# Optimization experiments

Hardware: AMD Instinct MI355X
Metric: run time of the kernel (lower is better)

The kernel has to match this reference:

```python
import jax, jax.numpy as jnp
import numpy as np

B, T, D, H, L = 32, 2048, 512, 512, 2
G = 4 * H


def _lstm_layer(x, h0, c0, Wih, Whh, bih, bhh):
    """Run one LSTM layer over time, vectorized across batch.

    x: [B, T, D_in]; h0, c0: [H] (shared initial state across batch, as in the
    original module where every batch element reuses the same `states[i]`).
    Returns (ys [B, T, H], hT [B, H], cT [B, H]).
    """
    b = x.shape[0]
    # Precompute the input contribution to the gates for all timesteps at once
    # (the only part that doesn't depend on the recurrence): [B, T, 4H]
    xg = jnp.einsum('btd,gd->btg', x, Wih) + (bih + bhh)
    h_init = jnp.broadcast_to(h0, (b, H))
    c_init = jnp.broadcast_to(c0, (b, H))

    def step(carry, xg_t):
        h, c = carry  # [B, H] each
        gates = xg_t + h @ Whh.T  # [B, 4H]
        i, f, g, o = jnp.split(gates, 4, axis=-1)  # torch LSTMCell gate order
        c = jax.nn.sigmoid(f) * c + jax.nn.sigmoid(i) * jnp.tanh(g)
        h = jax.nn.sigmoid(o) * jnp.tanh(c)
        return (h, c), h

    (hT, cT), ys = jax.lax.scan(step, (h_init, c_init), jnp.swapaxes(xg, 0, 1))
    return jnp.swapaxes(ys, 0, 1), hT, cT  # ys -> [B, T, H]


def setup_inputs() -> dict:
    key = jax.random.key(0)
    ks = jax.random.split(key, 9)
    s_in = 1.0 / np.sqrt(H)
    inp = {
        'x': jax.random.normal(ks[0], (B, T, D), jnp.float32),
        'Wih0': jax.random.normal(ks[1], (G, D), jnp.float32) * s_in,
        'Whh0': jax.random.normal(ks[2], (G, H), jnp.float32) * s_in,
        'bih0': jax.random.normal(ks[3], (G,), jnp.float32) * s_in,
        'bhh0': jax.random.normal(ks[4], (G,), jnp.float32) * s_in,
        'Wih1': jax.random.normal(ks[5], (G, H), jnp.float32) * s_in,
        'Whh1': jax.random.normal(ks[6], (G, H), jnp.float32) * s_in,
        'bih1': jax.random.normal(ks[7], (G,), jnp.float32) * s_in,
        'bhh1': jax.random.normal(ks[8], (G,), jnp.float32) * s_in,
        'h0': jnp.zeros((L, H), jnp.float32),
        'c0': jnp.zeros((L, H), jnp.float32),
    }
    return inp


def reference(x, Wih0, Whh0, bih0, bhh0, Wih1, Whh1, bih1, bhh1, h0, c0):
    # Layer 0
    y, h_f0, c_f0 = _lstm_layer(x, h0[0], c0[0], Wih0, Whh0, bih0, bhh0)
    # Layer 1 (no dropout: dropout_probability=None)
    y, h_f1, c_f1 = _lstm_layer(y, h0[1], c0[1], Wih1, Whh1, bih1, bhh1)
    h_final = jnp.stack([h_f0, h_f1])  # [L, B, H]
    c_final = jnp.stack([c_f0, c_f1])  # [L, B, H]
    return y, h_final, c_final
```

## Files before the change

### kernel.cpp

```cpp
#include <hip/hip_runtime.h>

namespace {
constexpr int TT   = 2048;
constexpr int NBLK = 128;
constexpr size_t YSZ = (size_t)32 * TT * 512;
constexpr size_t HFO = YSZ;
constexpr size_t CFO = YSZ + (size_t)2 * 32 * 512;
}

typedef float f32x4 __attribute__((ext_vector_type(4)));
typedef short s16x8 __attribute__((ext_vector_type(8)));

__device__ __forceinline__ float sigf(float v)  { return 1.0f / (1.0f + __expf(-v)); }
__device__ __forceinline__ float tanh_(float v) { return 1.0f - 2.0f / (__expf(2.0f * v) + 1.0f); }
__device__ __forceinline__ short f2bf(float v) {
  unsigned u = __float_as_uint(v);
  u += 0x7FFFu + ((u >> 16) & 1u);
  return (short)(u >> 16);
}
__device__ __forceinline__ float bf2f(short h) {
  return __uint_as_float(((unsigned)(unsigned short)h) << 16);
}
__device__ __forceinline__ void st_short_coh(void* p, int v) {
  asm volatile("global_store_short %0, %1, off sc1" :: "v"(p), "v"(v) : "memory");
}
__device__ __forceinline__ void poll2(const int* f, int need) {
  while (true) {
    const int a = __hip_atomic_load(f,      __ATOMIC_RELAXED, __HIP_MEMORY_SCOPE_AGENT);
    const int b = __hip_atomic_load(f + 64, __ATOMIC_RELAXED, __HIP_MEMORY_SCOPE_AGENT);
    if (a >= need && b >= need) break;
    __builtin_amdgcn_s_sleep(1);
  }
}

#define GLLP(g, l) __builtin_amdgcn_global_load_lds(                          \
    (const __attribute__((address_space(1))) void*)(g),                       \
    (__attribute__((address_space(3))) void*)(l), 16, 0, 0)
#define GLLC(g, l) __builtin_amdgcn_global_load_lds(                          \
    (const __attribute__((address_space(1))) void*)(g),                       \
    (__attribute__((address_space(3))) void*)(l), 16, 0, 0x11)

#define VMCNT0() do { asm volatile("s_waitcnt vmcnt(0)" ::: "memory"); __builtin_amdgcn_sched_barrier(0); } while (0)
#define LGKM0()  do { asm volatile("s_waitcnt lgkmcnt(0)" ::: "memory"); __builtin_amdgcn_sched_barrier(0); } while (0)
#define BAR()    do { __builtin_amdgcn_s_barrier(); __builtin_amdgcn_sched_barrier(0); } while (0)

__global__ __launch_bounds__(512)
void lstm_persist(
    const float* __restrict__ x,
    const float* __restrict__ Wih0, const float* __restrict__ Whh0,
    const float* __restrict__ bih0, const float* __restrict__ bhh0,
    const float* __restrict__ Wih1, const float* __restrict__ Whh1,
    const float* __restrict__ bih1, const float* __restrict__ bhh1,
    const float* __restrict__ h0c, const float* __restrict__ c0c,
    float* __restrict__ out,
    short* __restrict__ r0hi, short* __restrict__ r0lo,
    short* __restrict__ r1hi, short* __restrict__ r1lo,
    int* __restrict__ flags0, int* __restrict__ flags1)
{
  __shared__ __align__(16) short Whi[16 * 1024];
  __shared__ __align__(16) short Wlo[16 * 1024];
  __shared__ __align__(16) float stage[32 * 512];
  __shared__ __align__(16) float gbuf[16 * 33];
  __shared__ __align__(16) float xgb[2][16 * 33];

  const int tid   = (int)threadIdx.x;
  const int layer = (int)(blockIdx.x >> 7);
  const int lb    = (int)(blockIdx.x & (NBLK - 1));
  const int j0    = lb << 2;
  const int lane  = tid & 63;
  const int wg    = tid >> 6;
  char* stageb = (char*)stage;

  const float* Wih = layer ? Wih1 : Wih0;
  const float* Whh = layer ? Whh1 : Whh0;
  const float* bih = layer ? bih1 : bih0;
  const float* bhh = layer ? bhh1 : bhh0;
  short* rwhi = layer ? r1hi : r0hi;
  short* rwlo = layer ? r1lo : r0lo;
  int* fl_own = layer ? flags1 : flags0;
  const int awb = layer ? 0 : 512;
  const int bwb = layer ? 512 : 0;

  for (int idx = tid; idx < 16 * 1024; idx += 512) {
    const int row = idx >> 10;
    const int k   = idx & 1023;
    const int rg  = ((row >> 2) << 9) + j0 + (row & 3);
    const float v = (k < 512) ? Wih[(rg << 9) + k] : Whh[(rg << 9) + (k - 512)];
    const short h = f2bf(v);
    const short l = f2bf(v - bf2f(h));
    const int byte = (row << 11) + ((k << 1) ^ ((row & 7) << 4));
    *(short*)((char*)Whi + byte) = h;
    *(short*)((char*)Wlo + byte) = l;
  }
  float creg = 0.0f;
  float bias_[4] = {0.f, 0.f, 0.f, 0.f};
  if (tid < 128) {
    const int jj = tid & 3;
    creg = c0c[layer * 512 + j0 + jj];
#pragma unroll
    for (int g = 0; g < 4; ++g) {
      const int rg = (g << 9) + j0 + jj;
      bias_[g] = bih[rg] + bhh[rg];
    }
  }

  auto stage_planes = [&](const short* rh, const short* rl) {
#pragma unroll
    for (int i = 0; i < 4; ++i) {
      const int b = (i << 3) + wg;
      const int off = (b << 10) + ((lane << 4) ^ ((b & 7) << 4));
      GLLC((const char*)rh + off, stageb + (b << 10));
      GLLC((const char*)rl + off, stageb + 32768 + (b << 10));
    }
  };
  auto stage_x = [&](int sn) {
#pragma unroll
    for (int i = 0; i < 8; ++i) {
      const int u = (wg << 3) + i;
      const int b = u >> 1, half = (u & 1) << 10;
      const char* src = (const char*)x + ((size_t)(b * 2048 + sn) << 11) + half
                        + ((lane << 4) ^ ((b & 7) << 4));
      GLLP(src, stageb + (b << 11) + half);
    }
  };
  auto stage_bcast = [&](const float* p) {
#pragma unroll
    for (int i = 0; i < 8; ++i) {
      const int u = (wg << 3) + i;
      const int b = u >> 1, half = (u & 1) << 10;
      GLLP((const char*)p + half + ((lane << 4) ^ ((b & 7) << 4)),
           stageb + (b << 11) + half);
    }
  };

  auto do_mfma = [&](int wbase, bool cvt, float* dst) {
    f32x4 a0 = {0.f, 0.f, 0.f, 0.f}, a1 = {0.f, 0.f, 0.f, 0.f};
    const int arow = lane & 15;
    const int kg   = lane >> 4;
    const int bb   = (wg << 4) + (lane & 15);
    const int wsz  = (arow & 7) << 4;
    const int usz  = (bb & 7) << 4;
#pragma unroll
    for (int ks = 0; ks < 16; ++ks) {
      const int ku = ks * 32 + (kg << 3);
      const int wb = ((wbase + ku) << 1) ^ wsz;
      const s16x8 ah = *(const s16x8*)((const char*)Whi + (arow << 11) + wb);
      const s16x8 al = *(const s16x8*)((const char*)Wlo + (arow << 11) + wb);
      s16x8 bh, bl;
      if (!cvt) {
        const int ub = ((ku << 1) ^ usz);
        bh = *(const s16x8*)(stageb + (bb << 10) + ub);
        bl = *(const s16x8*)(stageb + 32768 + (bb << 10) + ub);
      } else {
        const f32x4 p = *(const f32x4*)(stageb + (bb << 11) + ((ku << 2) ^ usz));
        const f32x4 q = *(const f32x4*)(stageb + (bb << 11) + (((ku + 4) << 2) ^ usz));
        const float pv[8] = {p.x, p.y, p.z, p.w, q.x, q.y, q.z, q.w};
#pragma unroll
        for (int j = 0; j < 8; ++j) {
          const short h = f2bf(pv[j]);
          bh[j] = h;
          bl[j] = f2bf(pv[j] - bf2f(h));
        }
      }
      if (ks & 1) {
        a1 = __builtin_amdgcn_mfma_f32_16x16x32_bf16(ah, bh, a1, 0, 0, 0);
        a1 = __builtin_amdgcn_mfma_f32_16x16x32_bf16(ah, bl, a1, 0, 0, 0);
        a1 = __builtin_amdgcn_mfma_f32_16x16x32_bf16(al, bh, a1, 0, 0, 0);
      } else {
        a0 = __builtin_amdgcn_mfma_f32_16x16x32_bf16(ah, bh, a0, 0, 0, 0);
        a0 = __builtin_amdgcn_mfma_f32_16x16x32_bf16(ah, bl, a0, 0, 0, 0);
        a0 = __builtin_amdgcn_mfma_f32_16x16x32_bf16(al, bh, a0, 0, 0, 0);
      }
    }
    const f32x4 c = a0 + a1;
#pragma unroll
    for (int r = 0; r < 4; ++r)
      dst[((kg << 2) + r) * 33 + (wg << 4) + (lane & 15)] = c[r];
    LGKM0();
  };

  VMCNT0(); LGKM0(); BAR();

  if (layer == 0) stage_x(0); else stage_bcast(h0c + 512);
  VMCNT0(); BAR();
  if (wg < 2) do_mfma(bwb, true, &xgb[0][0]);
  if (layer == 1 && wg == 2) poll2(flags0 + lane, 1);
  BAR();
  if (layer == 0) stage_bcast(h0c);
  else            stage_planes(r0hi, r0lo);
  VMCNT0(); BAR();

#pragma unroll 1
  for (int s = 0; s < TT; ++s) {
    const int slot = s & 3;
    if (wg < 2) do_mfma(awb, layer == 0 && s == 0, gbuf);
    if (tid < 128) {
      const int jj = tid & 3;
      const int b  = tid >> 2;
      const float* xg = &xgb[s & 1][0];
      const float gi = gbuf[jj * 33 + b]        + xg[jj * 33 + b]        + bias_[0];
      const float gf = gbuf[(4 + jj) * 33 + b]  + xg[(4 + jj) * 33 + b]  + bias_[1];
      const float gg = gbuf[(8 + jj) * 33 + b]  + xg[(8 + jj) * 33 + b]  + bias_[2];
      const float go = gbuf[(12 + jj) * 33 + b] + xg[(12 + jj) * 33 + b] + bias_[3];
      const float cn = sigf(gf) * creg + sigf(gi) * tanh_(gg);
      const float hn = sigf(go) * tanh_(cn);
      creg = cn;
      const int j = j0 + jj;
      const short hb = f2bf(hn);
      const short lbh = f2bf(hn - bf2f(hb));
      short* ph = rwhi + (((slot << 5) + b) << 9) + j;
      short* pl = rwlo + (((slot << 5) + b) << 9) + j;
      st_short_coh(ph, (int)hb);
      st_short_coh(pl, (int)lbh);
      if (layer == 1) out[((size_t)((b << 11) + s) << 9) + j] = hn;
      if (s == TT - 1) out[HFO + (size_t)(((layer << 5) + b) << 9) + j] = hn;
      asm volatile("s_waitcnt vmcnt(0)" ::: "memory");
    }
    __builtin_amdgcn_sched_barrier(0);
    BAR();
    if (tid == 0)
      __hip_atomic_store(fl_own + lb, s + 1, __ATOMIC_RELAXED, __HIP_MEMORY_SCOPE_AGENT);

    if (s + 1 < TT) {
      if (layer == 1) {
        if (wg == 2) poll2(flags1 + lane, s + 1);
        BAR();
      }
      if (layer == 0) stage_x(s + 1);
      else            stage_planes(r1hi + (slot << 14), r1lo + (slot << 14));
      VMCNT0(); BAR();
      if (wg < 2) do_mfma(bwb, layer == 0, &xgb[(s + 1) & 1][0]);
      if (wg == 2) poll2(flags0 + lane, layer == 0 ? s + 1 : s + 2);
      if (wg == 3 && s >= 3) poll2(flags1 + lane, s - 2);
      BAR();
      if (layer == 0) stage_planes(r0hi + (slot << 14), r0lo + (slot << 14));
      else            stage_planes(r0hi + (((s + 1) & 3) << 14), r0lo + (((s + 1) & 3) << 14));
      VMCNT0(); BAR();
    }
  }

  if (tid < 128)
    out[CFO + (size_t)(((layer << 5) + (tid >> 2)) << 9) + j0 + (tid & 3)] = creg;
}

extern "C" void kernel_launch(void* const* d_in, const int* in_sizes, int n_in,
                              void* d_out, int out_size, void* d_ws, size_t ws_size,
                              hipStream_t stream) {
  (void)in_sizes; (void)n_in; (void)out_size; (void)ws_size;
  const float* x    = (const float*)d_in[0];
  const float* Wih0 = (const float*)d_in[1];
  const float* Whh0 = (const float*)d_in[2];
  const float* bih0 = (const float*)d_in[3];
  const float* bhh0 = (const float*)d_in[4];
  const float* Wih1 = (const float*)d_in[5];
  const float* Whh1 = (const float*)d_in[6];
  const float* bih1 = (const float*)d_in[7];
  const float* bhh1 = (const float*)d_in[8];
  const float* h0   = (const float*)d_in[9];
  const float* c0   = (const float*)d_in[10];

  float* out = (float*)d_out;
  short* r0hi = (short*)d_ws;
  short* r0lo = (short*)((char*)d_ws + (128 << 10));
  short* r1hi = (short*)((char*)d_ws + (256 << 10));
  short* r1lo = (short*)((char*)d_ws + (384 << 10));
  int* flags0 = (int*)((char*)d_ws + (512 << 10));
  int* flags1 = (int*)((char*)d_ws + (512 << 10) + 512);

  hipMemsetAsync(flags0, 0, 1024, stream);

  hipLaunchKernelGGL(lstm_persist, dim3(2 * NBLK), dim3(512), 0, stream,
                     x, Wih0, Whh0, bih0, bhh0, Wih1, Whh1, bih1, bhh1,
                     h0, c0, out, r0hi, r0lo, r1hi, r1lo, flags0, flags1);
}
```

Measured before the change: 16.70 ms.

## Split block into recurrent and input-projection wave groups with chunked double-buffered staging

Restructures the persistent LSTM kernel into 256-thread blocks where two waves compute only the recurrent h@Whh MFMA and two other waves compute the input projection and the gate nonlinearities. The input-projection waves stream x (or the layer-0 h planes) in eight k-chunks with double buffering and partial vmcnt waits, so loads overlap MFMA work. Per-wave flags replace per-block flags, which shortens the critical recurrent path. This raises LDS use to about 148KB and makes the synchronisation more intricate, with risk of added polling overhead.

```diff
diff --git a/kernel.cpp b/kernel.cpp
--- a/kernel.cpp
+++ b/kernel.cpp
@@ -6,6 +6,12 @@
 constexpr size_t YSZ = (size_t)32 * TT * 512;
 constexpr size_t HFO = YSZ;
 constexpr size_t CFO = YSZ + (size_t)2 * 32 * 512;
+constexpr int O_WLO = 32768;
+constexpr int O_AST = 65536;
+constexpr int O_B0  = 131072;
+constexpr int O_B1  = 139264;
+constexpr int O_GA  = 147456;
+constexpr int O_XGB = 149568;
 }
 
 typedef float f32x4 __attribute__((ext_vector_type(4)));
@@ -24,12 +30,20 @@
 __device__ __forceinline__ void st_short_coh(void* p, int v) {
   asm volatile("global_store_short %0, %1, off sc1" :: "v"(p), "v"(v) : "memory");
 }
-__device__ __forceinline__ void poll2(const int* f, int need) {
-  while (true) {
-    const int a = __hip_atomic_load(f,      __ATOMIC_RELAXED, __HIP_MEMORY_SCOPE_AGENT);
-    const int b = __hip_atomic_load(f + 64, __ATOMIC_RELAXED, __HIP_MEMORY_SCOPE_AGENT);
-    if (a >= need && b >= need) break;
+__device__ __forceinline__ void st_flag(int* p, int v) {
+  __hip_atomic_store(p, v, __ATOMIC_RELAXED, __HIP_MEMORY_SCOPE_AGENT);
+}
+__device__ __forceinline__ void poll_ge(const int* f, int need) {
+  while (__hip_atomic_load(f, __ATOMIC_RELAXED, __HIP_MEMORY_SCOPE_AGENT) < need)
     __builtin_amdgcn_s_sleep(1);
+}
+__device__ __forceinline__ void cvt8(const f32x4& p, const f32x4& q, s16x8& bh, s16x8& bl) {
+  const float pv[8] = {p.x, p.y, p.z, p.w, q.x, q.y, q.z, q.w};
+#pragma unroll
+  for (int j = 0; j < 8; ++j) {
+    const short h = f2bf(pv[j]);
+    bh[j] = h;
+    bl[j] = f2bf(pv[j] - bf2f(h));
   }
 }
 
@@ -40,11 +54,12 @@
     (const __attribute__((address_space(1))) void*)(g),                       \
     (__attribute__((address_space(3))) void*)(l), 16, 0, 0x11)
 
+#define VMCNT4() do { asm volatile("s_waitcnt vmcnt(4)" ::: "memory"); __builtin_amdgcn_sched_barrier(0); } while (0)
 #define VMCNT0() do { asm volatile("s_waitcnt vmcnt(0)" ::: "memory"); __builtin_amdgcn_sched_barrier(0); } while (0)
 #define LGKM0()  do { asm volatile("s_waitcnt lgkmcnt(0)" ::: "memory"); __builtin_amdgcn_sched_barrier(0); } while (0)
 #define BAR()    do { __builtin_amdgcn_s_barrier(); __builtin_amdgcn_sched_barrier(0); } while (0)
 
-__global__ __launch_bounds__(512)
+__global__ __launch_bounds__(256)
 void lstm_persist(
     const float* __restrict__ x,
     const float* __restrict__ Wih0, const float* __restrict__ Whh0,
@@ -57,190 +72,229 @@
     short* __restrict__ r1hi, short* __restrict__ r1lo,
     int* __restrict__ flags0, int* __restrict__ flags1)
 {
-  __shared__ __align__(16) short Whi[16 * 1024];
-  __shared__ __align__(16) short Wlo[16 * 1024];
-  __shared__ __align__(16) float stage[32 * 512];
-  __shared__ __align__(16) float gbuf[16 * 33];
-  __shared__ __align__(16) float xgb[2][16 * 33];
+  __shared__ __align__(16) char LDS[151680];
+  char* Whi = LDS;
+  char* Wlo = LDS + O_WLO;
+  char* Ast = LDS + O_AST;
+  char* const Bst0 = LDS + O_B0;
+  char* const Bst1 = LDS + O_B1;
+  float* gA  = (float*)(LDS + O_GA);
+  float* xgb = (float*)(LDS + O_XGB);
 
   const int tid   = (int)threadIdx.x;
+  const int lane  = tid & 63;
+  const int w     = tid >> 6;
   const int layer = (int)(blockIdx.x >> 7);
   const int lb    = (int)(blockIdx.x & (NBLK - 1));
   const int j0    = lb << 2;
-  const int lane  = tid & 63;
-  const int wg    = tid >> 6;
-  char* stageb = (char*)stage;
+  const bool isA  = (w < 2);
 
   const float* Wih = layer ? Wih1 : Wih0;
   const float* Whh = layer ? Whh1 : Whh0;
   const float* bih = layer ? bih1 : bih0;
   const float* bhh = layer ? bhh1 : bhh0;
-  short* rwhi = layer ? r1hi : r0hi;
-  short* rwlo = layer ? r1lo : r0lo;
-  int* fl_own = layer ? flags1 : flags0;
-  const int awb = layer ? 0 : 512;
-  const int bwb = layer ? 512 : 0;
-
-  for (int idx = tid; idx < 16 * 1024; idx += 512) {
+  short* rhiO = layer ? r1hi : r0hi;
+  short* rloO = layer ? r1lo : r0lo;
+  int* flO = layer ? flags1 : flags0;
+
+  for (int idx = tid; idx < 16 * 1024; idx += 256) {
     const int row = idx >> 10;
     const int k   = idx & 1023;
     const int rg  = ((row >> 2) << 9) + j0 + (row & 3);
     const float v = (k < 512) ? Wih[(rg << 9) + k] : Whh[(rg << 9) + (k - 512)];
     const short h = f2bf(v);
     const short l = f2bf(v - bf2f(h));
-    const int byte = (row << 11) + ((k << 1) ^ ((row & 7) << 4));
-    *(short*)((char*)Whi + byte) = h;
-    *(short*)((char*)Wlo + byte) = l;
+    const int byte = (row << 11) + ((k << 1) ^ ((row & 15) << 4));
+    *(short*)(Whi + byte) = h;
+    *(short*)(Wlo + byte) = l;
   }
   float creg = 0.0f;
   float bias_[4] = {0.f, 0.f, 0.f, 0.f};
-  if (tid < 128) {
-    const int jj = tid & 3;
-    creg = c0c[layer * 512 + j0 + jj];
+  int jjC = 0, bC = 0;
+  if (!isA) {
+    jjC = lane >> 4;
+    bC  = ((w - 2) << 4) + (lane & 15);
+    creg = c0c[layer * 512 + j0 + jjC];
 #pragma unroll
     for (int g = 0; g < 4; ++g) {
-      const int rg = (g << 9) + j0 + jj;
+      const int rg = (g << 9) + j0 + jjC;
       bias_[g] = bih[rg] + bhh[rg];
     }
   }
 
-  auto stage_planes = [&](const short* rh, const short* rl) {
-#pragma unroll
-    for (int i = 0; i < 4; ++i) {
-      const int b = (i << 3) + wg;
-      const int off = (b << 10) + ((lane << 4) ^ ((b & 7) << 4));
-      GLLC((const char*)rh + off, stageb + (b << 10));
-      GLLC((const char*)rl + off, stageb + 32768 + (b << 10));
+  const int arow = lane & 15;
+  const int kg   = lane >> 4;
+  const int wsz  = arow << 4;
+  const int bbA  = (w << 4) + (lane & 15);
+  const int uszA = (bbA & 15) << 4;
+  const int bbB  = ((w - 2) << 4) + (lane & 15);
+  const int uszB  = (bbB & 15) << 4;
+  const int uszB7 = (bbB & 7) << 4;
+
+  if (isA) {
+    const char* src0 = (const char*)(h0c + layer * 512);
+#pragma unroll 1
+    for (int i = 0; i < 32; ++i) {
+      const int g = (w << 5) + i;
+      const int b = g >> 1, half = g & 1;
+      GLLP(src0 + (half << 10) + ((lane << 4) ^ ((b & 15) << 4)),
+           Ast + (b << 11) + (half << 10));
     }
-  };
-  auto stage_x = [&](int sn) {
-#pragma unroll
-    for (int i = 0; i < 8; ++i) {
-      const int u = (wg << 3) + i;
-      const int b = u >> 1, half = (u & 1) << 10;
-      const char* src = (const char*)x + ((size_t)(b * 2048 + sn) << 11) + half
-                        + ((lane << 4) ^ ((b & 7) << 4));
-      GLLP(src, stageb + (b << 11) + half);
-    }
-  };
-  auto stage_bcast = [&](const float* p) {
-#pragma unroll
-    for (int i = 0; i < 8; ++i) {
-      const int u = (wg << 3) + i;
-      const int b = u >> 1, half = (u & 1) << 10;
-      GLLP((const char*)p + half + ((lane << 4) ^ ((b & 7) << 4)),
-           stageb + (b << 11) + half);
-    }
-  };
-
-  auto do_mfma = [&](int wbase, bool cvt, float* dst) {
-    f32x4 a0 = {0.f, 0.f, 0.f, 0.f}, a1 = {0.f, 0.f, 0.f, 0.f};
-    const int arow = lane & 15;
-    const int kg   = lane >> 4;
-    const int bb   = (wg << 4) + (lane & 15);
-    const int wsz  = (arow & 7) << 4;
-    const int usz  = (bb & 7) << 4;
-#pragma unroll
-    for (int ks = 0; ks < 16; ++ks) {
-      const int ku = ks * 32 + (kg << 3);
-      const int wb = ((wbase + ku) << 1) ^ wsz;
-      const s16x8 ah = *(const s16x8*)((const char*)Whi + (arow << 11) + wb);
-      const s16x8 al = *(const s16x8*)((const char*)Wlo + (arow << 11) + wb);
-      s16x8 bh, bl;
-      if (!cvt) {
-        const int ub = ((ku << 1) ^ usz);
-        bh = *(const s16x8*)(stageb + (bb << 10) + ub);
-        bl = *(const s16x8*)(stageb + 32768 + (bb << 10) + ub);
-      } else {
-        const f32x4 p = *(const f32x4*)(stageb + (bb << 11) + ((ku << 2) ^ usz));
-        const f32x4 q = *(const f32x4*)(stageb + (bb << 11) + (((ku + 4) << 2) ^ usz));
-        const float pv[8] = {p.x, p.y, p.z, p.w, q.x, q.y, q.z, q.w};
-#pragma unroll
-        for (int j = 0; j < 8; ++j) {
-          const short h = f2bf(pv[j]);
-          bh[j] = h;
-          bl[j] = f2bf(pv[j] - bf2f(h));
-        }
-      }
-      if (ks & 1) {
-        a1 = __builtin_amdgcn_mfma_f32_16x16x32_bf16(ah, bh, a1, 0, 0, 0);
-        a1 = __builtin_amdgcn_mfma_f32_16x16x32_bf16(ah, bl, a1, 0, 0, 0);
-        a1 = __builtin_amdgcn_mfma_f32_16x16x32_bf16(al, bh, a1, 0, 0, 0);
-      } else {
-        a0 = __builtin_amdgcn_mfma_f32_16x16x32_bf16(ah, bh, a0, 0, 0, 0);
-        a0 = __builtin_amdgcn_mfma_f32_16x16x32_bf16(ah, bl, a0, 0, 0, 0);
-        a0 = __builtin_amdgcn_mfma_f32_16x16x32_bf16(al, bh, a0, 0, 0, 0);
-      }
-    }
-    const f32x4 c = a0 + a1;
-#pragma unroll
-    for (int r = 0; r < 4; ++r)
-      dst[((kg << 2) + r) * 33 + (wg << 4) + (lane & 15)] = c[r];
-    LGKM0();
-  };
-
-  VMCNT0(); LGKM0(); BAR();
-
-  if (layer == 0) stage_x(0); else stage_bcast(h0c + 512);
-  VMCNT0(); BAR();
-  if (wg < 2) do_mfma(bwb, true, &xgb[0][0]);
-  if (layer == 1 && wg == 2) poll2(flags0 + lane, 1);
+    VMCNT0();
+  }
   BAR();
-  if (layer == 0) stage_bcast(h0c);
-  else            stage_planes(r0hi, r0lo);
-  VMCNT0(); BAR();
 
 #pragma unroll 1
   for (int s = 0; s < TT; ++s) {
     const int slot = s & 3;
-    if (wg < 2) do_mfma(awb, layer == 0 && s == 0, gbuf);
-    if (tid < 128) {
-      const int jj = tid & 3;
-      const int b  = tid >> 2;
-      const float* xg = &xgb[s & 1][0];
-      const float gi = gbuf[jj * 33 + b]        + xg[jj * 33 + b]        + bias_[0];
-      const float gf = gbuf[(4 + jj) * 33 + b]  + xg[(4 + jj) * 33 + b]  + bias_[1];
-      const float gg = gbuf[(8 + jj) * 33 + b]  + xg[(8 + jj) * 33 + b]  + bias_[2];
-      const float go = gbuf[(12 + jj) * 33 + b] + xg[(12 + jj) * 33 + b] + bias_[3];
-      const float cn = sigf(gf) * creg + sigf(gi) * tanh_(gg);
-      const float hn = sigf(go) * tanh_(cn);
+    if (isA) {
+      f32x4 a0 = {0.f,0.f,0.f,0.f}, a1 = {0.f,0.f,0.f,0.f};
+#pragma unroll
+      for (int ks = 0; ks < 16; ++ks) {
+        const int wk = 512 + (ks << 5) + (kg << 3);
+        const int wb = ((wk << 1) ^ wsz);
+        const s16x8 ah = *(const s16x8*)(Whi + (arow << 11) + wb);
+        const s16x8 al = *(const s16x8*)(Wlo + (arow << 11) + wb);
+        const int uk = (ks << 5) + (kg << 3);
+        s16x8 bh, bl;
+        if (s == 0) {
+          const f32x4 p = *(const f32x4*)(Ast + (bbA << 11) + ((uk << 2) ^ uszA));
+          const f32x4 q = *(const f32x4*)(Ast + (bbA << 11) + (((uk + 4) << 2) ^ uszA));
+          cvt8(p, q, bh, bl);
+        } else {
+          const int ub = (uk << 1) ^ uszA;
+          bh = *(const s16x8*)(Ast + (bbA << 10) + ub);
+          bl = *(const s16x8*)(Ast + 32768 + (bbA << 10) + ub);
+        }
+        if (ks & 1) {
+          a1 = __builtin_amdgcn_mfma_f32_16x16x32_bf16(ah, bh, a1, 0, 0, 0);
+          a1 = __builtin_amdgcn_mfma_f32_16x16x32_bf16(ah, bl, a1, 0, 0, 0);
+          a1 = __builtin_amdgcn_mfma_f32_16x16x32_bf16(al, bh, a1, 0, 0, 0);
+        } else {
+          a0 = __builtin_amdgcn_mfma_f32_16x16x32_bf16(ah, bh, a0, 0, 0, 0);
+          a0 = __builtin_amdgcn_mfma_f32_16x16x32_bf16(ah, bl, a0, 0, 0, 0);
+          a0 = __builtin_amdgcn_mfma_f32_16x16x32_bf16(al, bh, a0, 0, 0, 0);
+        }
+      }
+      const f32x4 c = a0 + a1;
+#pragma unroll
+      for (int r = 0; r < 4; ++r) gA[((kg << 2) + r) * 33 + bbA] = c[r];
+      LGKM0();
+      BAR();
+      if (s + 1 < TT) {
+        poll_ge(flO + tid, s + 1);
+        poll_ge(flO + 128 + tid, s + 1);
+        if (layer == 0 && s >= 3) {
+          poll_ge(flags1 + tid, s - 2);
+          poll_ge(flags1 + 128 + tid, s - 2);
+        }
+        const char* sp = (const char*)(w == 0 ? rhiO : rloO);
+#pragma unroll 1
+        for (int b = 0; b < 32; ++b) {
+          GLLC(sp + ((((slot << 5) + b) << 10)) + ((lane << 4) ^ ((b & 15) << 4)),
+               Ast + (w << 15) + (b << 10));
+        }
+        VMCNT0();
+      }
+      BAR();
+    } else {
+      if (layer == 1) {
+        poll_ge(flags0 + (tid - 128), s + 1);
+        poll_ge(flags0 + (tid - 128) + 128, s + 1);
+      }
+      const int bw = w - 2;
+      auto issueChunk = [&](char* buf, int c) {
+        if (layer == 0) {
+#pragma unroll
+          for (int j = 0; j < 4; ++j) {
+            const int b = (bw << 4) + (j << 2) + (lane >> 4);
+            const char* src = (const char*)x
+                + ((((size_t)b * 2048 + s) * 512 + ((size_t)c << 6)) << 2)
+                + (((lane & 15) << 4) ^ ((b & 15) << 4));
+            GLLP(src, buf + (((bw << 4) + (j << 2)) << 8));
+          }
+        } else {
+#pragma unroll
+          for (int j = 0; j < 4; ++j) {
+            const int hi = (j < 2);
+            const int b = (bw << 4) + ((j & 1) << 3) + (lane >> 3);
+            const char* rb = hi ? (const char*)r0hi : (const char*)r0lo;
+            const char* src = rb
+                + (((((size_t)slot << 5) + b) * 512 + ((size_t)c << 6)) << 1)
+                + (((lane & 7) << 4) ^ ((b & 7) << 4));
+            GLLC(src, buf + (hi ? 0 : 4096) + (((bw << 4) + ((j & 1) << 3)) << 7));
+          }
+        }
+      };
+      auto mfmaChunk = [&](const char* buf, int c, f32x4& a0, f32x4& a1) {
+#pragma unroll
+        for (int i = 0; i < 2; ++i) {
+          const int wk = (c << 6) + (i << 5) + (kg << 3);
+          const int wb = ((wk << 1) ^ wsz);
+          const s16x8 ah = *(const s16x8*)(Whi + (arow << 11) + wb);
+          const s16x8 al = *(const s16x8*)(Wlo + (arow << 11) + wb);
+          const int kk = (i << 5) + (kg << 3);
+          s16x8 bh, bl;
+          if (layer == 0) {
+            const f32x4 p = *(const f32x4*)(buf + (bbB << 8) + ((kk << 2) ^ uszB));
+            const f32x4 q = *(const f32x4*)(buf + (bbB << 8) + (((kk + 4) << 2) ^ uszB));
+            cvt8(p, q, bh, bl);
+          } else {
+            const int ub = (kk << 1) ^ uszB7;
+            bh = *(const s16x8*)(buf + (bbB << 7) + ub);
+            bl = *(const s16x8*)(buf + 4096 + (bbB << 7) + ub);
+          }
+          if (i & 1) {
+            a1 = __builtin_amdgcn_mfma_f32_16x16x32_bf16(ah, bh, a1, 0, 0, 0);
+            a1 = __builtin_amdgcn_mfma_f32_16x16x32_bf16(ah, bl, a1, 0, 0, 0);
+            a1 = __builtin_amdgcn_mfma_f32_16x16x32_bf16(al, bh, a1, 0, 0, 0);
+          } else {
+            a0 = __builtin_amdgcn_mfma_f32_16x16x32_bf16(ah, bh, a0, 0, 0, 0);
+            a0 = __builtin_amdgcn_mfma_f32_16x16x32_bf16(ah, bl, a0, 0, 0, 0);
+            a0 = __builtin_amdgcn_mfma_f32_16x16x32_bf16(al, bh, a0, 0, 0, 0);
+          }
+        }
+      };
+      f32x4 a0 = {0.f,0.f,0.f,0.f}, a1 = {0.f,0.f,0.f,0.f};
+      issueChunk(Bst0, 0);
+      issueChunk(Bst1, 1);
+#pragma unroll 1
+      for (int c = 0; c < 8; ++c) {
+        if (c == 7) { VMCNT0(); } else { VMCNT4(); }
+        char* buf = (c & 1) ? Bst1 : Bst0;
+        mfmaChunk(buf, c, a0, a1);
+        __builtin_amdgcn_sched_barrier(0);
+        if (c < 6) issueChunk(buf, c + 2);
+      }
+      BAR();
+      const f32x4 cf = a0 + a1;
+#pragma unroll
+      for (int r = 0; r < 4; ++r) xgb[((kg << 2) + r) * 33 + bbB] = cf[r];
+      LGKM0();
+      float gv[4];
+#pragma unroll
+      for (int g = 0; g < 4; ++g) {
+        const int rowi = ((g << 2) + jjC) * 33 + bC;
+        gv[g] = gA[rowi] + xgb[rowi] + bias_[g];
+      }
+      const float cn = sigf(gv[1]) * creg + sigf(gv[0]) * tanh_(gv[2]);
+      const float hn = sigf(gv[3]) * tanh_(cn);
       creg = cn;
-      const int j = j0 + jj;
+      const int j = j0 + jjC;
       const short hb = f2bf(hn);
-      const short lbh = f2bf(hn - bf2f(hb));
-      short* ph = rwhi + (((slot << 5) + b) << 9) + j;
-      short* pl = rwlo + (((slot << 5) + b) << 9) + j;
-      st_short_coh(ph, (int)hb);
-      st_short_coh(pl, (int)lbh);
-      if (layer == 1) out[((size_t)((b << 11) + s) << 9) + j] = hn;
-      if (s == TT - 1) out[HFO + (size_t)(((layer << 5) + b) << 9) + j] = hn;
-      asm volatile("s_waitcnt vmcnt(0)" ::: "memory");
+      const short lo2 = f2bf(hn - bf2f(hb));
+      st_short_coh(rhiO + (((slot << 5) + bC) << 9) + j, (int)hb);
+      st_short_coh(rloO + (((slot << 5) + bC) << 9) + j, (int)lo2);
+      if (layer == 1) out[(((size_t)bC * 2048 + s) << 9) + j] = hn;
+      if (s == TT - 1) out[HFO + (size_t)(((layer << 5) + bC) << 9) + j] = hn;
+      VMCNT0();
+      if (lane == 0) st_flag(flO + (lb << 1) + (w - 2), s + 1);
+      BAR();
     }
-    __builtin_amdgcn_sched_barrier(0);
-    BAR();
-    if (tid == 0)
-      __hip_atomic_store(fl_own + lb, s + 1, __ATOMIC_RELAXED, __HIP_MEMORY_SCOPE_AGENT);
-
-    if (s + 1 < TT) {
-      if (layer == 1) {
-        if (wg == 2) poll2(flags1 + lane, s + 1);
-        BAR();
-      }
-      if (layer == 0) stage_x(s + 1);
-      else            stage_planes(r1hi + (slot << 14), r1lo + (slot << 14));
-      VMCNT0(); BAR();
-      if (wg < 2) do_mfma(bwb, layer == 0, &xgb[(s + 1) & 1][0]);
-      if (wg == 2) poll2(flags0 + lane, layer == 0 ? s + 1 : s + 2);
-      if (wg == 3 && s >= 3) poll2(flags1 + lane, s - 2);
-      BAR();
-      if (layer == 0) stage_planes(r0hi + (slot << 14), r0lo + (slot << 14));
-      else            stage_planes(r0hi + (((s + 1) & 3) << 14), r0lo + (((s + 1) & 3) << 14));
-      VMCNT0(); BAR();
-    }
-  }
-
-  if (tid < 128)
-    out[CFO + (size_t)(((layer << 5) + (tid >> 2)) << 9) + j0 + (tid & 3)] = creg;
+  }
+
+  if (!isA)
+    out[CFO + (size_t)(((layer << 5) + bC) << 9) + j0 + jjC] = creg;
 }
 
 extern "C" void kernel_launch(void* const* d_in, const int* in_sizes, int n_in,
@@ -265,11 +319,11 @@
   short* r1hi = (short*)((char*)d_ws + (256 << 10));
   short* r1lo = (short*)((char*)d_ws + (384 << 10));
   int* flags0 = (int*)((char*)d_ws + (512 << 10));
-  int* flags1 = (int*)((char*)d_ws + (512 << 10) + 512);
-
-  hipMemsetAsync(flags0, 0, 1024, stream);
-
-  hipLaunchKernelGGL(lstm_persist, dim3(2 * NBLK), dim3(512), 0, stream,
+  int* flags1 = (int*)((char*)d_ws + (512 << 10) + 1024);
+
+  hipMemsetAsync(flags0, 0, 2048, stream);
+
+  hipLaunchKernelGGL(lstm_persist, dim3(2 * NBLK), dim3(256), 0, stream,
                      x, Wih0, Whh0, bih0, bhh0, Wih1, Whh1, bih1, bhh1,
                      h0, c0, out, r0hi, r0lo, r1hi, r1lo, flags0, flags1);
 }
```

New measurement: 24.54 ms. 47.0% more time.
